# Optimization experiments

Measured on AMD Instinct MI355X. Metric: run time of the kernel, lower is better.

## Reference

```python
import jax, jax.numpy as jnp
import numpy as np

DIM = 64
NUM_HEADS = 2
HEAD_DIM = DIM // NUM_HEADS


def setup_inputs() -> dict:
    key = jax.random.key(0)
    k1, k2, k3 = jax.random.split(key, 3)
    b, c, h, w = 8, DIM, 256, 256
    x = jax.random.normal(k1, (b, c, h, w), dtype=jnp.float32)
    # 1x1 conv weights, stored as [out_ch, in_ch] (kernel spatial dims are 1)
    qkv_w = jax.random.normal(k2, (3 * c, c), dtype=jnp.float32) * (1.0 / np.sqrt(c))
    proj_w = jax.random.normal(k3, (c, c), dtype=jnp.float32) * (1.0 / np.sqrt(c))
    return {"x": x, "qkv_w": qkv_w, "proj_w": proj_w}


def _phi(t):
    # elu(x) + 1 feature map (positive-valued kernel features)
    return jax.nn.elu(t) + 1.0


def reference(x, qkv_w, proj_w):
    b, c, h, w = x.shape
    n = h * w
    # 1x1 conv == per-pixel channel matmul
    qkv = jnp.einsum('oc,bchw->bohw', qkv_w, x)  # [b, 3c, h, w]
    q, k, v = jnp.split(qkv, 3, axis=1)

    def reshape(t):
        return t.reshape(b, NUM_HEADS, HEAD_DIM, n)  # bhcn

    q_phi = _phi(reshape(q))
    k_phi = _phi(reshape(k))
    v_h = reshape(v)
    # KV outer product over the sequence dim: tiny [b, h, c, d]
    KV = jnp.einsum('bhcn,bhdn->bhcd', k_phi, v_h)
    out_h = jnp.einsum('bhcn,bhcd->bhdn', q_phi, KV)  # [b, h, d, n]
    out = out_h.reshape(b, c, h, w)
    return jnp.einsum('oc,bchw->bohw', proj_w, out)
```

## Files before the change

### kernel.cpp

```cpp
#include <hip/hip_runtime.h>
#include <hip/hip_bf16.h>

#define BATCH 8
#define CH    64
#define NPIX  65536
#define NHEAD 2
#define HDIM  32
#define P1_BLOCKS 128

typedef __attribute__((ext_vector_type(8))) short bf16x8;
typedef __attribute__((ext_vector_type(4))) short bf16x4;
typedef __attribute__((ext_vector_type(4))) float f32x4;

#define MFMA32(a, b, c) __builtin_amdgcn_mfma_f32_16x16x32_bf16(a, b, c, 0, 0, 0)

#if __has_builtin(__builtin_amdgcn_mfma_f32_16x16x16_bf16)
typedef __attribute__((ext_vector_type(4))) __bf16 bf16v4;
#define MFMA16(a, b, c) __builtin_amdgcn_mfma_f32_16x16x16_bf16( \
    __builtin_bit_cast(bf16v4, (a)), __builtin_bit_cast(bf16v4, (b)), (c), 0, 0, 0)
#else
#define MFMA16(a, b, c) __builtin_amdgcn_mfma_f32_16x16x16bf16_1k((a), (b), (c), 0, 0, 0)
#endif

__device__ __forceinline__ unsigned rne_pk(float lo, float hi) {
    unsigned ua = __float_as_uint(lo); ua += 0x7fffu + ((ua >> 16) & 1u);
    unsigned ub = __float_as_uint(hi); ub += 0x7fffu + ((ub >> 16) & 1u);
    return (ua >> 16) | (ub & 0xffff0000u);
}

__device__ __forceinline__ bf16x8 pack8(const float* f) {
    int4 iv;
    iv.x = (int)rne_pk(f[0], f[1]);
    iv.y = (int)rne_pk(f[2], f[3]);
    iv.z = (int)rne_pk(f[4], f[5]);
    iv.w = (int)rne_pk(f[6], f[7]);
    return *reinterpret_cast<bf16x8*>(&iv);
}

__device__ __forceinline__ float phi_f(float t) {
    return t > 0.0f ? t + 1.0f : __expf(t);
}

__device__ __forceinline__ bf16x8 load_w_frag(const float* W, int r0, int k0, int lane) {
    const float* p = W + (size_t)(r0 + (lane & 15)) * 64 + k0 + ((lane >> 4) << 3);
    float f[8];
    #pragma unroll
    for (int e = 0; e < 8; e++) f[e] = p[e];
    return pack8(f);
}

__global__ __launch_bounds__(256) void la_pass1(
    const float* __restrict__ x, const float* __restrict__ qkv_w,
    float* __restrict__ partials, unsigned short* __restrict__ xt)
{
    __shared__ __align__(16) unsigned char smem[33024];
    unsigned short* xls = (unsigned short*)smem;

    const int tid  = threadIdx.x;
    const int lane = tid & 63;
    const int wv   = __builtin_amdgcn_readfirstlane(tid >> 6);
    const int b    = blockIdx.y;
    const int g    = lane >> 4;
    const int li   = lane & 15;

    bf16x8 Wf[8][2];
    #pragma unroll
    for (int j = 0; j < 8; j++)
        #pragma unroll
        for (int ks = 0; ks < 2; ks++)
            Wf[j][ks] = load_w_frag(qkv_w, 64 + 16 * j, 32 * ks, lane);

    f32x4 kvacc[2][2][2];
    #pragma unroll
    for (int h = 0; h < 2; h++)
        #pragma unroll
        for (int m2 = 0; m2 < 2; m2++)
            #pragma unroll
            for (int nt = 0; nt < 2; nt++)
                kvacc[h][m2][nt] = (f32x4){0.f, 0.f, 0.f, 0.f};

    const float* xb = x + (size_t)b * CH * NPIX;
    unsigned short* xtb = xt + (size_t)b * NPIX * CH;

    for (int it = 0; it < 2; it++) {
        const int px0 = (blockIdx.x * 2 + it) * 256;

        #pragma unroll
        for (int k4 = 0; k4 < 4; k4++) {
            float4 f[4];
            #pragma unroll
            for (int k = 0; k < 4; k++)
                f[k] = *reinterpret_cast<const float4*>(
                    xb + (size_t)(wv + 4 * (4 * k4 + k)) * NPIX + px0 + 4 * lane);
            #pragma unroll
            for (int k = 0; k < 4; k++)
                *reinterpret_cast<uint2*>(&xls[(wv + 4 * (4 * k4 + k)) * 258 + 4 * lane]) =
                    make_uint2(rne_pk(f[k].x, f[k].y), rne_pk(f[k].z, f[k].w));
        }
        __syncthreads();

        #pragma unroll
        for (int mt = 0; mt < 4; mt++) {
            const int pxl = 64 * wv + 16 * mt + li;

            bf16x8 xa[2];
            #pragma unroll
            for (int ks = 0; ks < 2; ks++) {
                unsigned v[8];
                #pragma unroll
                for (int e = 0; e < 8; e++)
                    v[e] = xls[(32 * ks + 8 * g + e) * 258 + pxl];
                int4 iv;
                iv.x = (int)(v[0] | (v[1] << 16));
                iv.y = (int)(v[2] | (v[3] << 16));
                iv.z = (int)(v[4] | (v[5] << 16));
                iv.w = (int)(v[6] | (v[7] << 16));
                xa[ks] = *reinterpret_cast<bf16x8*>(&iv);
            }

            bf16x4 kA[4], vB[4];
            #pragma unroll
            for (int j = 0; j < 8; j++) {
                f32x4 acc = (f32x4){0.f, 0.f, 0.f, 0.f};
                acc = MFMA32(xa[0], Wf[j][0], acc);
                acc = MFMA32(xa[1], Wf[j][1], acc);
                float v0 = acc[0], v1 = acc[1], v2 = acc[2], v3 = acc[3];
                if (j < 4) { v0 = phi_f(v0); v1 = phi_f(v1); v2 = phi_f(v2); v3 = phi_f(v3); }
                uint2 p = make_uint2(rne_pk(v0, v1), rne_pk(v2, v3));
                bf16x4 r = __builtin_bit_cast(bf16x4, p);
                if (j < 4) kA[j] = r; else vB[j - 4] = r;
            }

            #pragma unroll
            for (int h = 0; h < 2; h++)
                #pragma unroll
                for (int m2 = 0; m2 < 2; m2++)
                    #pragma unroll
                    for (int nt = 0; nt < 2; nt++)
                        kvacc[h][m2][nt] = MFMA16(kA[2 * h + m2], vB[2 * h + nt], kvacc[h][m2][nt]);
        }

        #pragma unroll
        for (int seg = 0; seg < 4; seg++) {
            const int pxl = 64 * seg + (tid >> 2);
            const int c0  = (tid & 3) * 16;
            unsigned d[8];
            #pragma unroll
            for (int i = 0; i < 8; i++) {
                unsigned lo = xls[(c0 + 2 * i) * 258 + pxl];
                unsigned hi = xls[(c0 + 2 * i + 1) * 258 + pxl];
                d[i] = lo | (hi << 16);
            }
            unsigned short* dst = xtb + (size_t)(px0 + pxl) * CH + c0;
            int4 lo4; lo4.x = (int)d[0]; lo4.y = (int)d[1]; lo4.z = (int)d[2]; lo4.w = (int)d[3];
            int4 hi4; hi4.x = (int)d[4]; hi4.y = (int)d[5]; hi4.z = (int)d[6]; hi4.w = (int)d[7];
            *reinterpret_cast<int4*>(dst)     = lo4;
            *reinterpret_cast<int4*>(dst + 8) = hi4;
        }
        __syncthreads();
    }

    float* rbuf = (float*)smem;
    #pragma unroll
    for (int h = 0; h < 2; h++)
        #pragma unroll
        for (int m2 = 0; m2 < 2; m2++)
            #pragma unroll
            for (int nt = 0; nt < 2; nt++) {
                const int t = (h * 2 + m2) * 2 + nt;
                #pragma unroll
                for (int r = 0; r < 4; r++)
                    rbuf[wv * 2048 + t * 256 + (4 * g + r) * 16 + li] = kvacc[h][m2][nt][r];
            }
    __syncthreads();

    float* outp = partials + ((size_t)b * P1_BLOCKS + blockIdx.x) * 2048;
    #pragma unroll
    for (int i = 0; i < 8; i++) {
        const int idx = i * 256 + tid;
        const float sum = rbuf[idx] + rbuf[2048 + idx] + rbuf[4096 + idx] + rbuf[6144 + idx];
        const int t = idx >> 8, within = idx & 255;
        const int row = within >> 4, col = within & 15;
        const int h = t >> 2, m2 = (t >> 1) & 1, nt = t & 1;
        outp[(h * 32 + 16 * m2 + row) * 32 + 16 * nt + col] = sum;
    }
}

__global__ __launch_bounds__(256) void la_reduce(
    const float* __restrict__ partials, float* __restrict__ kv)
{
    const int b = blockIdx.x >> 3;
    const int e = (blockIdx.x & 7) * 256 + threadIdx.x;
    const float* p = partials + (size_t)b * P1_BLOCKS * 2048 + e;
    float s0 = 0.f, s1 = 0.f, s2 = 0.f, s3 = 0.f;
    #pragma unroll 8
    for (int j = 0; j < P1_BLOCKS; j += 4) {
        s0 += p[(size_t)j * 2048];
        s1 += p[(size_t)(j + 1) * 2048];
        s2 += p[(size_t)(j + 2) * 2048];
        s3 += p[(size_t)(j + 3) * 2048];
    }
    kv[(size_t)b * 2048 + e] = (s0 + s1) + (s2 + s3);
}

__global__ __launch_bounds__(256) void la_pass2(
    const unsigned short* __restrict__ xt, const float* __restrict__ qkv_w,
    const float* __restrict__ proj_w, const float* __restrict__ kv,
    float* __restrict__ y)
{
    __shared__ __align__(16) unsigned short sm2[4][2][16][72];

    const int tid  = threadIdx.x;
    const int lane = tid & 63;
    const int wv   = __builtin_amdgcn_readfirstlane(tid >> 6);
    const int b    = blockIdx.y;
    const int g    = lane >> 4;
    const int li   = lane & 15;

    unsigned short* qT = &sm2[wv][0][0][0];
    unsigned short* oT = &sm2[wv][1][0][0];

    bf16x8 Aq[4][2], Ap[4][2], Akv[2][2];
    #pragma unroll
    for (int mt = 0; mt < 4; mt++)
        #pragma unroll
        for (int ks = 0; ks < 2; ks++) {
            Aq[mt][ks] = load_w_frag(qkv_w, 16 * mt, 32 * ks, lane);
            Ap[mt][ks] = load_w_frag(proj_w, 16 * mt, 32 * ks, lane);
        }
    const float* kvb = kv + (size_t)b * NHEAD * HDIM * HDIM;
    #pragma unroll
    for (int h = 0; h < 2; h++)
        #pragma unroll
        for (int mtd = 0; mtd < 2; mtd++) {
            float f[8];
            #pragma unroll
            for (int e = 0; e < 8; e++)
                f[e] = kvb[h * 1024 + (8 * g + e) * 32 + 16 * mtd + li];
            Akv[h][mtd] = pack8(f);
        }

    const unsigned short* xtb = xt + (size_t)b * NPIX * CH;
    float*                yb  = y  + (size_t)b * CH * NPIX;

    for (int s = blockIdx.x * 4 + wv; s < 4096; s += 1024) {
        const int px0 = s * 16;

        bf16x8 bx[2];
        const unsigned short* xp = xtb + (size_t)(px0 + li) * CH + 8 * g;
        bx[0] = *reinterpret_cast<const bf16x8*>(xp);
        bx[1] = *reinterpret_cast<const bf16x8*>(xp + 32);

        #pragma unroll
        for (int mt = 0; mt < 4; mt++) {
            f32x4 acc = (f32x4){0.f, 0.f, 0.f, 0.f};
            acc = MFMA32(Aq[mt][0], bx[0], acc);
            acc = MFMA32(Aq[mt][1], bx[1], acc);
            const float p0 = phi_f(acc[0]), p1 = phi_f(acc[1]);
            const float p2 = phi_f(acc[2]), p3 = phi_f(acc[3]);
            *reinterpret_cast<uint2*>(qT + li * 72 + 16 * mt + 4 * g) =
                make_uint2(rne_pk(p0, p1), rne_pk(p2, p3));
        }

        #pragma unroll
        for (int h = 0; h < 2; h++) {
            const bf16x8 bq = *reinterpret_cast<const bf16x8*>(qT + li * 72 + 32 * h + 8 * g);
            #pragma unroll
            for (int mtd = 0; mtd < 2; mtd++) {
                f32x4 acc = (f32x4){0.f, 0.f, 0.f, 0.f};
                acc = MFMA32(Akv[h][mtd], bq, acc);
                *reinterpret_cast<uint2*>(oT + li * 72 + 32 * h + 16 * mtd + 4 * g) =
                    make_uint2(rne_pk(acc[0], acc[1]), rne_pk(acc[2], acc[3]));
            }
        }

        const bf16x8 bo0 = *reinterpret_cast<const bf16x8*>(oT + li * 72 + 8 * g);
        const bf16x8 bo1 = *reinterpret_cast<const bf16x8*>(oT + li * 72 + 32 + 8 * g);
        #pragma unroll
        for (int mt = 0; mt < 4; mt++) {
            f32x4 acc = (f32x4){0.f, 0.f, 0.f, 0.f};
            acc = MFMA32(Ap[mt][0], bo0, acc);
            acc = MFMA32(Ap[mt][1], bo1, acc);
            #pragma unroll
            for (int r = 0; r < 4; r++)
                __builtin_nontemporal_store(acc[r],
                    &yb[(size_t)(16 * mt + 4 * g + r) * NPIX + px0 + li]);
        }
    }
}

extern "C" void kernel_launch(void* const* d_in, const int* in_sizes, int n_in,
                              void* d_out, int out_size, void* d_ws, size_t ws_size,
                              hipStream_t stream) {
    (void)in_sizes; (void)n_in; (void)out_size; (void)ws_size;
    const float* x      = (const float*)d_in[0];
    const float* qkv_w  = (const float*)d_in[1];
    const float* proj_w = (const float*)d_in[2];
    float* yout = (float*)d_out;

    unsigned short* xtw      = (unsigned short*)d_ws;
    float*          partials = (float*)(xtw + (size_t)BATCH * NPIX * CH);
    float*          kv       = partials + (size_t)BATCH * P1_BLOCKS * 2048;

    la_pass1 <<<dim3(P1_BLOCKS, BATCH), dim3(256), 0, stream>>>(x, qkv_w, partials, xtw);
    la_reduce<<<dim3(64),               dim3(256), 0, stream>>>(partials, kv);
    la_pass2 <<<dim3(256, BATCH),       dim3(256), 0, stream>>>(xtw, qkv_w, proj_w, kv, yout);
}
```

Before: 125.5 us.

## Drop bf16 transposed x staging; read fp32 x directly in both passes

Pass1 no longer stages x through LDS or writes a transposed bf16 copy to the workspace. Each wave now loads its MFMA fragments straight from global fp32 x with strided per-channel loads, and the block count doubles so every wave covers 4 tiles of 16 pixels. Pass2 rereads fp32 x directly instead of the bf16 transposed copy. This removes the 64 MB intermediate write and trades it for twice as many bytes read of x in pass2, plus less-coalesced 64-byte segment loads and no LDS reuse.

New measurement: 136.0 us. 8.4% more time.

```diff
diff --git a/kernel.cpp b/kernel.cpp
--- a/kernel.cpp
+++ b/kernel.cpp
@@ -6,7 +6,7 @@
 #define NPIX  65536
 #define NHEAD 2
 #define HDIM  32
-#define P1_BLOCKS 128
+#define P1_BLOCKS 256
 
 typedef __attribute__((ext_vector_type(8))) short bf16x8;
 typedef __attribute__((ext_vector_type(4))) short bf16x4;
@@ -51,10 +51,9 @@
 
 __global__ __launch_bounds__(256) void la_pass1(
     const float* __restrict__ x, const float* __restrict__ qkv_w,
-    float* __restrict__ partials, unsigned short* __restrict__ xt)
+    float* __restrict__ partials)
 {
-    __shared__ __align__(16) unsigned char smem[33024];
-    unsigned short* xls = (unsigned short*)smem;
+    __shared__ __align__(16) float rbuf[4 * 2048];
 
     const int tid  = threadIdx.x;
     const int lane = tid & 63;
@@ -80,87 +79,44 @@
                 kvacc[h][m2][nt] = (f32x4){0.f, 0.f, 0.f, 0.f};
 
     const float* xb = x + (size_t)b * CH * NPIX;
-    unsigned short* xtb = xt + (size_t)b * NPIX * CH;
-
-    for (int it = 0; it < 2; it++) {
-        const int px0 = (blockIdx.x * 2 + it) * 256;
-
-        #pragma unroll
-        for (int k4 = 0; k4 < 4; k4++) {
-            float4 f[4];
-            #pragma unroll
-            for (int k = 0; k < 4; k++)
-                f[k] = *reinterpret_cast<const float4*>(
-                    xb + (size_t)(wv + 4 * (4 * k4 + k)) * NPIX + px0 + 4 * lane);
-            #pragma unroll
-            for (int k = 0; k < 4; k++)
-                *reinterpret_cast<uint2*>(&xls[(wv + 4 * (4 * k4 + k)) * 258 + 4 * lane]) =
-                    make_uint2(rne_pk(f[k].x, f[k].y), rne_pk(f[k].z, f[k].w));
-        }
-        __syncthreads();
-
-        #pragma unroll
-        for (int mt = 0; mt < 4; mt++) {
-            const int pxl = 64 * wv + 16 * mt + li;
-
-            bf16x8 xa[2];
-            #pragma unroll
-            for (int ks = 0; ks < 2; ks++) {
-                unsigned v[8];
+    const int wid = blockIdx.x * 4 + wv;
+
+    for (int i = 0; i < 4; i++) {
+        const int px0 = (wid + i * 1024) * 16;
+
+        bf16x8 xa[2];
+        const float* xp = xb + px0 + li;
+        #pragma unroll
+        for (int ks = 0; ks < 2; ks++) {
+            float f[8];
+            #pragma unroll
+            for (int e = 0; e < 8; e++)
+                f[e] = xp[(size_t)(32 * ks + 8 * g + e) * NPIX];
+            xa[ks] = pack8(f);
+        }
+
+        bf16x4 kA[4], vB[4];
+        #pragma unroll
+        for (int j = 0; j < 8; j++) {
+            f32x4 acc = (f32x4){0.f, 0.f, 0.f, 0.f};
+            acc = MFMA32(xa[0], Wf[j][0], acc);
+            acc = MFMA32(xa[1], Wf[j][1], acc);
+            float v0 = acc[0], v1 = acc[1], v2 = acc[2], v3 = acc[3];
+            if (j < 4) { v0 = phi_f(v0); v1 = phi_f(v1); v2 = phi_f(v2); v3 = phi_f(v3); }
+            uint2 p = make_uint2(rne_pk(v0, v1), rne_pk(v2, v3));
+            bf16x4 r = __builtin_bit_cast(bf16x4, p);
+            if (j < 4) kA[j] = r; else vB[j - 4] = r;
+        }
+
+        #pragma unroll
+        for (int h = 0; h < 2; h++)
+            #pragma unroll
+            for (int m2 = 0; m2 < 2; m2++)
                 #pragma unroll
-                for (int e = 0; e < 8; e++)
-                    v[e] = xls[(32 * ks + 8 * g + e) * 258 + pxl];
-                int4 iv;
-                iv.x = (int)(v[0] | (v[1] << 16));
-                iv.y = (int)(v[2] | (v[3] << 16));
-                iv.z = (int)(v[4] | (v[5] << 16));
-                iv.w = (int)(v[6] | (v[7] << 16));
-                xa[ks] = *reinterpret_cast<bf16x8*>(&iv);
-            }
-
-            bf16x4 kA[4], vB[4];
-            #pragma unroll
-            for (int j = 0; j < 8; j++) {
-                f32x4 acc = (f32x4){0.f, 0.f, 0.f, 0.f};
-                acc = MFMA32(xa[0], Wf[j][0], acc);
-                acc = MFMA32(xa[1], Wf[j][1], acc);
-                float v0 = acc[0], v1 = acc[1], v2 = acc[2], v3 = acc[3];
-                if (j < 4) { v0 = phi_f(v0); v1 = phi_f(v1); v2 = phi_f(v2); v3 = phi_f(v3); }
-                uint2 p = make_uint2(rne_pk(v0, v1), rne_pk(v2, v3));
-                bf16x4 r = __builtin_bit_cast(bf16x4, p);
-                if (j < 4) kA[j] = r; else vB[j - 4] = r;
-            }
-
-            #pragma unroll
-            for (int h = 0; h < 2; h++)
-                #pragma unroll
-                for (int m2 = 0; m2 < 2; m2++)
-                    #pragma unroll
-                    for (int nt = 0; nt < 2; nt++)
-                        kvacc[h][m2][nt] = MFMA16(kA[2 * h + m2], vB[2 * h + nt], kvacc[h][m2][nt]);
-        }
-
-        #pragma unroll
-        for (int seg = 0; seg < 4; seg++) {
-            const int pxl = 64 * seg + (tid >> 2);
-            const int c0  = (tid & 3) * 16;
-            unsigned d[8];
-            #pragma unroll
-            for (int i = 0; i < 8; i++) {
-                unsigned lo = xls[(c0 + 2 * i) * 258 + pxl];
-                unsigned hi = xls[(c0 + 2 * i + 1) * 258 + pxl];
-                d[i] = lo | (hi << 16);
-            }
-            unsigned short* dst = xtb + (size_t)(px0 + pxl) * CH + c0;
-            int4 lo4; lo4.x = (int)d[0]; lo4.y = (int)d[1]; lo4.z = (int)d[2]; lo4.w = (int)d[3];
-            int4 hi4; hi4.x = (int)d[4]; hi4.y = (int)d[5]; hi4.z = (int)d[6]; hi4.w = (int)d[7];
-            *reinterpret_cast<int4*>(dst)     = lo4;
-            *reinterpret_cast<int4*>(dst + 8) = hi4;
-        }
-        __syncthreads();
-    }
-
-    float* rbuf = (float*)smem;
+                for (int nt = 0; nt < 2; nt++)
+                    kvacc[h][m2][nt] = MFMA16(kA[2 * h + m2], vB[2 * h + nt], kvacc[h][m2][nt]);
+    }
+
     #pragma unroll
     for (int h = 0; h < 2; h++)
         #pragma unroll
@@ -204,7 +160,7 @@
 }
 
 __global__ __launch_bounds__(256) void la_pass2(
-    const unsigned short* __restrict__ xt, const float* __restrict__ qkv_w,
+    const float* __restrict__ x, const float* __restrict__ qkv_w,
     const float* __restrict__ proj_w, const float* __restrict__ kv,
     float* __restrict__ y)
 {
@@ -240,16 +196,22 @@
             Akv[h][mtd] = pack8(f);
         }
 
-    const unsigned short* xtb = xt + (size_t)b * NPIX * CH;
-    float*                yb  = y  + (size_t)b * CH * NPIX;
+    const float* xb = x + (size_t)b * CH * NPIX;
+    float*       yb = y + (size_t)b * CH * NPIX;
 
     for (int s = blockIdx.x * 4 + wv; s < 4096; s += 1024) {
         const int px0 = s * 16;
 
         bf16x8 bx[2];
-        const unsigned short* xp = xtb + (size_t)(px0 + li) * CH + 8 * g;
-        bx[0] = *reinterpret_cast<const bf16x8*>(xp);
-        bx[1] = *reinterpret_cast<const bf16x8*>(xp + 32);
+        const float* xp = xb + px0 + li;
+        #pragma unroll
+        for (int ks = 0; ks < 2; ks++) {
+            float f[8];
+            #pragma unroll
+            for (int e = 0; e < 8; e++)
+                f[e] = xp[(size_t)(32 * ks + 8 * g + e) * NPIX];
+            bx[ks] = pack8(f);
+        }
 
         #pragma unroll
         for (int mt = 0; mt < 4; mt++) {
@@ -298,11 +260,10 @@
     const float* proj_w = (const float*)d_in[2];
     float* yout = (float*)d_out;
 
-    unsigned short* xtw      = (unsigned short*)d_ws;
-    float*          partials = (float*)(xtw + (size_t)BATCH * NPIX * CH);
-    float*          kv       = partials + (size_t)BATCH * P1_BLOCKS * 2048;
-
-    la_pass1 <<<dim3(P1_BLOCKS, BATCH), dim3(256), 0, stream>>>(x, qkv_w, partials, xtw);
+    float* partials = (float*)d_ws;
+    float* kv       = partials + (size_t)BATCH * P1_BLOCKS * 2048;
+
+    la_pass1 <<<dim3(P1_BLOCKS, BATCH), dim3(256), 0, stream>>>(x, qkv_w, partials);
     la_reduce<<<dim3(64),               dim3(256), 0, stream>>>(partials, kv);
-    la_pass2 <<<dim3(256, BATCH),       dim3(256), 0, stream>>>(xtw, qkv_w, proj_w, kv, yout);
-}
+    la_pass2 <<<dim3(256, BATCH),       dim3(256), 0, stream>>>(x, qkv_w, proj_w, kv, yout);
+}
```
